# Optimization experiments

Measured on AMD Instinct MI355X. Metric: run time of the kernel, lower is better.

The kernel has to match this reference:

```python
import jax, jax.numpy as jnp
import numpy as np

NUM_HOPS = 3
SIGMA = 0.1
EPS = 1e-12  # torch F.normalize default eps


def setup_inputs() -> dict:
    key = jax.random.key(0)
    k1, k2 = jax.random.split(key)
    N, D, E = 50000, 128, 800000
    x = jax.random.normal(k1, (N, D), dtype=jnp.float32)
    edge_index = jax.random.randint(k2, (2, E), 0, N, dtype=jnp.int64)
    return {"x": x, "edge_index": edge_index}


def _l2_normalize(h):
    # matches torch.nn.functional.normalize(x, dim=1)
    n = jnp.linalg.norm(h, axis=1, keepdims=True)
    return h / jnp.maximum(n, EPS)


def reference(x, edge_index):
    N = x.shape[0]
    src, dst = edge_index[0], edge_index[1]
    noise_keys = jax.random.split(jax.random.key(1), NUM_HOPS)

    h = _l2_normalize(x)
    outs = [h]
    for k in range(NUM_HOPS):
        # edge-wise inner-product similarity + sigmoid gate
        e = jnp.sum(h[src] * h[dst], axis=1)          # [E]
        alpha = jax.nn.sigmoid(e)                     # [E]
        # sparse alpha^T @ h == segment-sum over dst of alpha * h[src]
        aggr = jax.ops.segment_sum(alpha[:, None] * h[src], dst, num_segments=N)  # [N, D]
        noised = aggr + SIGMA * jax.random.normal(noise_keys[k], aggr.shape, dtype=x.dtype)
        h = _l2_normalize(noised)
        outs.append(h)
    return jnp.stack(outs)                            # [NUM_HOPS+1, N, D]
```

## Files before the change

### kernel.cpp

```cpp
#include <hip/hip_runtime.h>
#include <cstdint>
#include <cstddef>

#define D 128

__host__ __device__ inline uint32_t rotl32(uint32_t v, int d) {
  return (v << d) | (v >> (32 - d));
}

__host__ __device__ inline void threefry2x32(uint32_t k0, uint32_t k1,
                                             uint32_t x0, uint32_t x1,
                                             uint32_t* o0, uint32_t* o1) {
  uint32_t k2 = k0 ^ k1 ^ 0x1BD11BDAu;
  x0 += k0; x1 += k1;
#define TF_RND(r) x0 += x1; x1 = rotl32(x1, (r)); x1 ^= x0;
  TF_RND(13) TF_RND(15) TF_RND(26) TF_RND(6)
  x0 += k1; x1 += k2 + 1u;
  TF_RND(17) TF_RND(29) TF_RND(16) TF_RND(24)
  x0 += k2; x1 += k0 + 2u;
  TF_RND(13) TF_RND(15) TF_RND(26) TF_RND(6)
  x0 += k0; x1 += k1 + 3u;
  TF_RND(17) TF_RND(29) TF_RND(16) TF_RND(24)
  x0 += k1; x1 += k2 + 4u;
  TF_RND(13) TF_RND(15) TF_RND(26) TF_RND(6)
  x0 += k2; x1 += k0 + 5u;
#undef TF_RND
  *o0 = x0; *o1 = x1;
}

__device__ inline float erfinv_f32(float x) {
  float w = -log1pf(-x * x);
  float p;
  if (w < 5.0f) {
    w = w - 2.5f;
    p = 2.81022636e-08f;
    p = fmaf(p, w, 3.43273939e-07f);
    p = fmaf(p, w, -3.5233877e-06f);
    p = fmaf(p, w, -4.39150654e-06f);
    p = fmaf(p, w, 0.00021858087f);
    p = fmaf(p, w, -0.00125372503f);
    p = fmaf(p, w, -0.00417768164f);
    p = fmaf(p, w, 0.246640727f);
    p = fmaf(p, w, 1.50140941f);
  } else {
    w = sqrtf(w) - 3.0f;
    p = -0.000200214257f;
    p = fmaf(p, w, 0.000100950558f);
    p = fmaf(p, w, 0.00134934322f);
    p = fmaf(p, w, -0.00367342844f);
    p = fmaf(p, w, 0.00573950773f);
    p = fmaf(p, w, -0.0076224613f);
    p = fmaf(p, w, 0.00943887047f);
    p = fmaf(p, w, 1.00167406f);
    p = fmaf(p, w, 2.83297682f);
  }
  return p * x;
}

__device__ inline float jax_normal_elem(uint32_t k0, uint32_t k1, uint32_t idx) {
  uint32_t o0, o1;
  threefry2x32(k0, k1, 0u, idx, &o0, &o1);
  uint32_t bits = o0 ^ o1;
  float f = __uint_as_float((bits >> 9) | 0x3F800000u) - 1.0f;
  float u = f * 2.0f + (-0.99999994f);
  u = fmaxf(-0.99999994f, u);
  return 1.41421356237309505f * erfinv_f32(u);
}

__device__ inline uint32_t f32_to_bf16_rne(float f) {
  uint32_t u = __float_as_uint(f);
  u += 0x7fffu + ((u >> 16) & 1u);
  return u >> 16;
}

__global__ __launch_bounds__(256) void hist4_kernel(
    const int* __restrict__ dst, int* __restrict__ counts,
    int* __restrict__ deg_hist, int E4, int E) {
  if (blockIdx.x == 0) {
    for (int b = threadIdx.x; b < 1024; b += 256) deg_hist[b] = 0;
  }
  int t = blockIdx.x * blockDim.x + threadIdx.x;
  if (t < E4) {
    int4 d = ((const int4*)dst)[t];
    atomicAdd(&counts[d.x], 1);
    atomicAdd(&counts[d.y], 1);
    atomicAdd(&counts[d.z], 1);
    atomicAdd(&counts[d.w], 1);
  }
  int rem = E4 * 4 + t;
  if (t < E - E4 * 4) atomicAdd(&counts[dst[rem]], 1);
}

__global__ __launch_bounds__(256) void scanA_kernel(
    int* __restrict__ counts, int* __restrict__ blocksums,
    int* __restrict__ deg, int* __restrict__ deg_hist, int N) {
  __shared__ int tmp[256];
  __shared__ int lhist[1024];
  for (int b = threadIdx.x; b < 1024; b += 256) lhist[b] = 0;
  int tid = threadIdx.x;
  int i = blockIdx.x * 256 + tid;
  int v = (i < N) ? counts[i] : 0;
  tmp[tid] = v;
  __syncthreads();
  if (i < N) {
    deg[i] = v;
    atomicAdd(&lhist[min(v, 1023)], 1);
  }
  for (int off = 1; off < 256; off <<= 1) {
    int t = (tid >= off) ? tmp[tid - off] : 0;
    __syncthreads();
    tmp[tid] += t;
    __syncthreads();
  }
  if (i < N) counts[i] = tmp[tid] - v;
  if (tid == 255) blocksums[blockIdx.x] = tmp[tid];
  __syncthreads();
  for (int b = threadIdx.x; b < 1024; b += 256) {
    int c = lhist[b];
    if (c) atomicAdd(&deg_hist[b], c);
  }
}

__global__ __launch_bounds__(256) void scanB_kernel(
    int* __restrict__ blocksums, int nb,
    const int* __restrict__ deg_hist, int* __restrict__ deg_cursor) {
  __shared__ int tmp[256];
  int tid = threadIdx.x;
  int v = (tid < nb) ? blocksums[tid] : 0;
  tmp[tid] = v;
  __syncthreads();
  for (int off = 1; off < 256; off <<= 1) {
    int t = (tid >= off) ? tmp[tid - off] : 0;
    __syncthreads();
    tmp[tid] += t;
    __syncthreads();
  }
  if (tid < nb) blocksums[tid] = tmp[tid] - v;
  __syncthreads();
  int loc[4], s = 0;
#pragma unroll
  for (int k = 0; k < 4; ++k) { loc[k] = deg_hist[tid * 4 + k]; s += loc[k]; }
  __syncthreads();
  tmp[tid] = s;
  __syncthreads();
  for (int off = 1; off < 256; off <<= 1) {
    int t = (tid >= off) ? tmp[tid - off] : 0;
    __syncthreads();
    tmp[tid] += t;
    __syncthreads();
  }
  int run = tmp[tid] - s;
#pragma unroll
  for (int k = 0; k < 4; ++k) { deg_cursor[tid * 4 + k] = run; run += loc[k]; }
}

__global__ __launch_bounds__(256) void scanC_kernel(
    int* __restrict__ offsets, int* __restrict__ cursor,
    const int* __restrict__ blocksums, const int* __restrict__ deg,
    int* __restrict__ deg_cursor, int* __restrict__ perm, int N, int E) {
  __shared__ int lhist[1024];
  __shared__ int lbase[1024];
  for (int b = threadIdx.x; b < 1024; b += 256) lhist[b] = 0;
  __syncthreads();
  int i = blockIdx.x * 256 + threadIdx.x;
  int d = 0, lpos = 0;
  if (i < N) {
    int o = offsets[i] + blocksums[blockIdx.x];
    offsets[i] = o;
    cursor[i] = o;
    d = min(deg[i], 1023);
    lpos = atomicAdd(&lhist[d], 1);
  }
  if (i == 0) offsets[N] = E;
  __syncthreads();
  for (int b = threadIdx.x; b < 1024; b += 256) {
    int c = lhist[b];
    lbase[b] = c ? atomicAdd(&deg_cursor[b], c) : 0;
  }
  __syncthreads();
  if (i < N) perm[lbase[d] + lpos] = i;
}

__global__ __launch_bounds__(256) void edgescatter4_kernel(
    const int* __restrict__ src, const int* __restrict__ dst,
    int* __restrict__ cursor, int* __restrict__ sorted_src, int E4, int E) {
  int t = blockIdx.x * blockDim.x + threadIdx.x;
  if (t < E4) {
    int4 d = ((const int4*)dst)[t];
    int4 s = ((const int4*)src)[t];
    sorted_src[atomicAdd(&cursor[d.x], 1)] = s.x;
    sorted_src[atomicAdd(&cursor[d.y], 1)] = s.y;
    sorted_src[atomicAdd(&cursor[d.z], 1)] = s.z;
    sorted_src[atomicAdd(&cursor[d.w], 1)] = s.w;
  }
  int rem = E4 * 4 + t;
  if (t < E - E4 * 4) {
    int d = dst[rem];
    sorted_src[atomicAdd(&cursor[d], 1)] = src[rem];
  }
}

__global__ __launch_bounds__(256) void norm_kernel(
    const float* __restrict__ in, float* __restrict__ out,
    uint16_t* __restrict__ mir, int N) {
  int t = blockIdx.x * blockDim.x + threadIdx.x;
  int row = t >> 6;
  int lane = t & 63;
  if (row >= N) return;
  size_t base = (size_t)row * D + 2 * lane;
  float2 v = *(const float2*)(in + base);
  float ss = v.x * v.x + v.y * v.y;
#pragma unroll
  for (int off = 32; off > 0; off >>= 1) ss += __shfl_xor(ss, off);
  float denom = fmaxf(sqrtf(ss), 1e-12f);
  float2 o = make_float2(v.x / denom, v.y / denom);
  *(float2*)(out + base) = o;
  if (mir) {
    uint32_t w = f32_to_bf16_rne(o.x) | (f32_to_bf16_rne(o.y) << 16);
    *(uint32_t*)(mir + base) = w;
  }
}

union V8 { float4 v[2]; float f[8]; };
union U4B { uint4 v; uint32_t u[4]; };

__device__ inline void hop_edge(const U4B& raw, const V8& b, V8& acc) {
  V8 af;
#pragma unroll
  for (int i = 0; i < 4; ++i) {
    af.f[2 * i] = __uint_as_float(raw.u[i] << 16);
    af.f[2 * i + 1] = __uint_as_float(raw.u[i] & 0xffff0000u);
  }
  float part = af.f[0] * b.f[0];
#pragma unroll
  for (int q = 1; q < 8; ++q) part = fmaf(af.f[q], b.f[q], part);
  part += __shfl_xor(part, 1);
  part += __shfl_xor(part, 2);
  part += __shfl_xor(part, 4);
  part += __shfl_xor(part, 8);
  float alpha = __builtin_amdgcn_rcpf(1.0f + __expf(-part));
#pragma unroll
  for (int q = 0; q < 8; ++q) acc.f[q] = fmaf(alpha, af.f[q], acc.f[q]);
}

__global__ __launch_bounds__(256, 4) void hop_kernel_bf16(
    const float* __restrict__ hprev, const uint16_t* __restrict__ mprev,
    float* __restrict__ hout, uint16_t* __restrict__ mout,
    const int* __restrict__ offsets, const int* __restrict__ sorted_src,
    const int* __restrict__ perm, int N, int E, uint32_t k0, uint32_t k1) {
  int g = (blockIdx.x * blockDim.x + threadIdx.x) >> 4;
  int sub = threadIdx.x & 15;
  if (g >= N) return;
  int r = perm[g];
  size_t rbase = (size_t)r * D + sub * 8;

  V8 b;
  {
    const float4* p = (const float4*)(hprev + rbase);
    b.v[0] = p[0]; b.v[1] = p[1];
  }
  V8 acc;
#pragma unroll
  for (int i = 0; i < 8; ++i) acc.f[i] = 0.f;

  int j0 = offsets[r];
  int cnt = offsets[r + 1] - j0;
  int Em1 = E - 1;
  const uint16_t* mp = mprev + sub * 8;

  U4B buf[4];
  int sNext[4];
#pragma unroll
  for (int q = 0; q < 4; ++q) {
    int s = sorted_src[min(j0 + q, Em1)];
    buf[q].v = *(const uint4*)(mp + (size_t)s * D);
  }
#pragma unroll
  for (int q = 0; q < 4; ++q) sNext[q] = sorted_src[min(j0 + 4 + q, Em1)];

  int cnt4 = cnt & ~3;
  int i = 0;
  for (; i < cnt4; i += 4) {
#pragma unroll
    for (int q = 0; q < 4; ++q) {
      hop_edge(buf[q], b, acc);
      buf[q].v = *(const uint4*)(mp + (size_t)sNext[q] * D);
      sNext[q] = sorted_src[min(j0 + i + 8 + q, Em1)];
    }
  }
  int rem = cnt - cnt4;
#pragma unroll
  for (int q = 0; q < 3; ++q)
    if (q < rem) hop_edge(buf[q], b, acc);

  uint32_t idx = (uint32_t)rbase;
  float ss = 0.f;
#pragma unroll
  for (int i2 = 0; i2 < 8; ++i2) {
    acc.f[i2] += 0.1f * jax_normal_elem(k0, k1, idx + (uint32_t)i2);
    ss = fmaf(acc.f[i2], acc.f[i2], ss);
  }
  ss += __shfl_xor(ss, 1);
  ss += __shfl_xor(ss, 2);
  ss += __shfl_xor(ss, 4);
  ss += __shfl_xor(ss, 8);
  float denom = fmaxf(sqrtf(ss), 1e-12f);
#pragma unroll
  for (int i2 = 0; i2 < 8; ++i2) acc.f[i2] = acc.f[i2] / denom;
  {
    float4* p = (float4*)(hout + rbase);
    p[0] = acc.v[0]; p[1] = acc.v[1];
  }
  if (mout) {
    U4B w;
#pragma unroll
    for (int i2 = 0; i2 < 4; ++i2)
      w.u[i2] = f32_to_bf16_rne(acc.f[2 * i2]) |
                (f32_to_bf16_rne(acc.f[2 * i2 + 1]) << 16);
    *(uint4*)(mout + rbase) = w.v;
  }
}

union V16 { float4 v[4]; float f[16]; };

__global__ __launch_bounds__(256) void hop_kernel_f32(
    const float* __restrict__ hprev, float* __restrict__ hout,
    const int* __restrict__ offsets, const int* __restrict__ sorted_src,
    const int* __restrict__ perm, int N, uint32_t k0, uint32_t k1) {
  int g = (blockIdx.x * blockDim.x + threadIdx.x) >> 3;
  int sub = threadIdx.x & 7;
  if (g >= N) return;
  int r = perm[g];
  size_t rbase = (size_t)r * D + sub * 16;

  V16 b;
  {
    const float4* p = (const float4*)(hprev + rbase);
    b.v[0] = p[0]; b.v[1] = p[1]; b.v[2] = p[2]; b.v[3] = p[3];
  }
  V16 acc;
#pragma unroll
  for (int i = 0; i < 16; ++i) acc.f[i] = 0.f;

  int j = offsets[r], jhi = offsets[r + 1];
  V16 a;
  if (j < jhi) {
    const float4* p = (const float4*)(hprev + (size_t)sorted_src[j] * D + sub * 16);
    a.v[0] = p[0]; a.v[1] = p[1]; a.v[2] = p[2]; a.v[3] = p[3];
  }
  while (j < jhi) {
    int jn = j + 1;
    V16 an;
    if (jn < jhi) {
      const float4* p = (const float4*)(hprev + (size_t)sorted_src[jn] * D + sub * 16);
      an.v[0] = p[0]; an.v[1] = p[1]; an.v[2] = p[2]; an.v[3] = p[3];
    }
    float part = a.f[0] * b.f[0];
#pragma unroll
    for (int i = 1; i < 16; ++i) part = fmaf(a.f[i], b.f[i], part);
    part += __shfl_xor(part, 1);
    part += __shfl_xor(part, 2);
    part += __shfl_xor(part, 4);
    float alpha = 1.0f / (1.0f + expf(-part));
#pragma unroll
    for (int i = 0; i < 16; ++i) acc.f[i] = fmaf(alpha, a.f[i], acc.f[i]);
    a = an;
    j = jn;
  }

  uint32_t idx = (uint32_t)rbase;
  float ss = 0.f;
#pragma unroll
  for (int i = 0; i < 16; ++i) {
    acc.f[i] += 0.1f * jax_normal_elem(k0, k1, idx + (uint32_t)i);
    ss = fmaf(acc.f[i], acc.f[i], ss);
  }
  ss += __shfl_xor(ss, 1);
  ss += __shfl_xor(ss, 2);
  ss += __shfl_xor(ss, 4);
  float denom = fmaxf(sqrtf(ss), 1e-12f);
#pragma unroll
  for (int i = 0; i < 16; ++i) acc.f[i] = acc.f[i] / denom;
  {
    float4* p = (float4*)(hout + rbase);
    p[0] = acc.v[0]; p[1] = acc.v[1]; p[2] = acc.v[2]; p[3] = acc.v[3];
  }
}

extern "C" void kernel_launch(void* const* d_in, const int* in_sizes, int n_in,
                              void* d_out, int out_size, void* d_ws, size_t ws_size,
                              hipStream_t stream) {
  const float* x = (const float*)d_in[0];
  const int* ei = (const int*)d_in[1];
  int N = in_sizes[0] / D;
  int E = in_sizes[1] / 2;
  const int* src = ei;
  const int* dst = ei + E;
  float* out = (float*)d_out;
  size_t ND = (size_t)N * D;

  int nblocksN = (N + 255) / 256;

  int* offsets = (int*)d_ws;
  int* cursor = offsets + (N + 1);
  int* perm = cursor + N;
  int* deg = perm + N;
  int* deg_hist = deg + N;
  int* deg_cursor = deg_hist + 1024;
  int* blocksums = deg_cursor + 1024;
  int* sorted_src = blocksums + 256;
  size_t intWords = (size_t)(N + 1) + N + N + N + 1024 + 1024 + 256 + E;
  size_t mirOff = (intWords * 4 + 255) & ~(size_t)255;
  size_t need = mirOff + 2 * ND * sizeof(uint16_t);
  bool use_bf16 = ws_size >= need;
  uint16_t* mir0 = (uint16_t*)((char*)d_ws + mirOff);
  uint16_t* mir1 = mir0 + ND;

  uint32_t nk0[3], nk1[3];
  for (int k = 0; k < 3; ++k)
    threefry2x32(0u, 1u, 0u, (uint32_t)k, &nk0[k], &nk1[k]);

  int E4 = E / 4;
  int e4Blocks = (max(E4, E - E4 * 4) + 255) / 256;
  int rowWaveBlocks = (int)(((size_t)N * 64 + 255) / 256);
  int hopBlocks16 = (int)(((size_t)N * 16 + 255) / 256);
  int hopBlocks8 = (int)(((size_t)N * 8 + 255) / 256);

  hipMemsetAsync(offsets, 0, (size_t)(N + 1) * sizeof(int), stream);
  hipLaunchKernelGGL(hist4_kernel, dim3(e4Blocks), dim3(256), 0, stream,
                     dst, offsets, deg_hist, E4, E);
  hipLaunchKernelGGL(scanA_kernel, dim3(nblocksN), dim3(256), 0, stream,
                     offsets, blocksums, deg, deg_hist, N);
  hipLaunchKernelGGL(scanB_kernel, dim3(1), dim3(256), 0, stream,
                     blocksums, nblocksN, deg_hist, deg_cursor);
  hipLaunchKernelGGL(scanC_kernel, dim3(nblocksN), dim3(256), 0, stream,
                     offsets, cursor, blocksums, deg, deg_cursor, perm, N, E);
  hipLaunchKernelGGL(edgescatter4_kernel, dim3(e4Blocks), dim3(256), 0, stream,
                     src, dst, cursor, sorted_src, E4, E);

  hipLaunchKernelGGL(norm_kernel, dim3(rowWaveBlocks), dim3(256), 0, stream,
                     x, out, use_bf16 ? mir0 : (uint16_t*)nullptr, N);

  if (use_bf16) {
    uint16_t* mirs[4] = {mir0, mir1, mir0, nullptr};
    for (int k = 0; k < 3; ++k) {
      const float* hk = out + (size_t)k * ND;
      float* hk1 = out + (size_t)(k + 1) * ND;
      hipLaunchKernelGGL(hop_kernel_bf16, dim3(hopBlocks16), dim3(256), 0, stream,
                         hk, mirs[k], hk1, mirs[k + 1], offsets, sorted_src,
                         perm, N, E, nk0[k], nk1[k]);
    }
  } else {
    for (int k = 0; k < 3; ++k) {
      const float* hk = out + (size_t)k * ND;
      float* hk1 = out + (size_t)(k + 1) * ND;
      hipLaunchKernelGGL(hop_kernel_f32, dim3(hopBlocks8), dim3(256), 0, stream,
                         hk, hk1, offsets, sorted_src, perm, N, nk0[k], nk1[k]);
    }
  }
}
```

Baseline: 390.0 us.

## Fuse input normalization into histogram kernel and micro-optimize bf16 hop kernel

```diff
diff --git a/kernel.cpp b/kernel.cpp
--- a/kernel.cpp
+++ b/kernel.cpp
@@ -3,6 +3,8 @@
 #include <cstddef>
 
 #define D 128
+
+typedef float v2f __attribute__((ext_vector_type(2)));
 
 __host__ __device__ inline uint32_t rotl32(uint32_t v, int d) {
   return (v << d) | (v >> (32 - d));
@@ -57,6 +59,36 @@
   return p * x;
 }
 
+__device__ inline float erfinv_fast(float x) {
+  float t = fmaf(-x, x, 1.0f);
+  float w = -0.693147180559945f * __builtin_amdgcn_logf(t);
+  float p;
+  if (__builtin_expect(w < 5.0f, 1)) {
+    w = w - 2.5f;
+    p = 2.81022636e-08f;
+    p = fmaf(p, w, 3.43273939e-07f);
+    p = fmaf(p, w, -3.5233877e-06f);
+    p = fmaf(p, w, -4.39150654e-06f);
+    p = fmaf(p, w, 0.00021858087f);
+    p = fmaf(p, w, -0.00125372503f);
+    p = fmaf(p, w, -0.00417768164f);
+    p = fmaf(p, w, 0.246640727f);
+    p = fmaf(p, w, 1.50140941f);
+  } else {
+    w = __builtin_amdgcn_sqrtf(w) - 3.0f;
+    p = -0.000200214257f;
+    p = fmaf(p, w, 0.000100950558f);
+    p = fmaf(p, w, 0.00134934322f);
+    p = fmaf(p, w, -0.00367342844f);
+    p = fmaf(p, w, 0.00573950773f);
+    p = fmaf(p, w, -0.0076224613f);
+    p = fmaf(p, w, 0.00943887047f);
+    p = fmaf(p, w, 1.00167406f);
+    p = fmaf(p, w, 2.83297682f);
+  }
+  return p * x;
+}
+
 __device__ inline float jax_normal_elem(uint32_t k0, uint32_t k1, uint32_t idx) {
   uint32_t o0, o1;
   threefry2x32(k0, k1, 0u, idx, &o0, &o1);
@@ -67,28 +99,60 @@
   return 1.41421356237309505f * erfinv_f32(u);
 }
 
+__device__ inline float jax_normal_fast(uint32_t k0, uint32_t k1, uint32_t idx) {
+  uint32_t o0, o1;
+  threefry2x32(k0, k1, 0u, idx, &o0, &o1);
+  uint32_t bits = o0 ^ o1;
+  float f = __uint_as_float((bits >> 9) | 0x3F800000u) - 1.0f;
+  float u = f * 2.0f + (-0.99999994f);
+  u = fmaxf(-0.99999994f, u);
+  return 1.41421356237309505f * erfinv_fast(u);
+}
+
 __device__ inline uint32_t f32_to_bf16_rne(float f) {
   uint32_t u = __float_as_uint(f);
   u += 0x7fffu + ((u >> 16) & 1u);
   return u >> 16;
 }
 
-__global__ __launch_bounds__(256) void hist4_kernel(
+__global__ __launch_bounds__(256) void front_kernel(
     const int* __restrict__ dst, int* __restrict__ counts,
-    int* __restrict__ deg_hist, int E4, int E) {
-  if (blockIdx.x == 0) {
-    for (int b = threadIdx.x; b < 1024; b += 256) deg_hist[b] = 0;
-  }
-  int t = blockIdx.x * blockDim.x + threadIdx.x;
-  if (t < E4) {
-    int4 d = ((const int4*)dst)[t];
-    atomicAdd(&counts[d.x], 1);
-    atomicAdd(&counts[d.y], 1);
-    atomicAdd(&counts[d.z], 1);
-    atomicAdd(&counts[d.w], 1);
-  }
-  int rem = E4 * 4 + t;
-  if (t < E - E4 * 4) atomicAdd(&counts[dst[rem]], 1);
+    int* __restrict__ deg_hist, int E4, int E,
+    const float* __restrict__ xin, float* __restrict__ out0,
+    uint16_t* __restrict__ mir, int N, int nbHist) {
+  int w = blockIdx.x;
+  if (w < nbHist) {
+    if (w == 0) {
+      for (int bb = threadIdx.x; bb < 1024; bb += 256) deg_hist[bb] = 0;
+    }
+    int t = w * 256 + threadIdx.x;
+    if (t < E4) {
+      int4 d4 = ((const int4*)dst)[t];
+      atomicAdd(&counts[d4.x], 1);
+      atomicAdd(&counts[d4.y], 1);
+      atomicAdd(&counts[d4.z], 1);
+      atomicAdd(&counts[d4.w], 1);
+    }
+    int rem = E4 * 4 + t;
+    if (t < E - E4 * 4) atomicAdd(&counts[dst[rem]], 1);
+    return;
+  }
+  int t = (w - nbHist) * 256 + threadIdx.x;
+  int row = t >> 6;
+  int lane = t & 63;
+  if (row >= N) return;
+  size_t base = (size_t)row * D + 2 * lane;
+  float2 v = *(const float2*)(xin + base);
+  float ss = v.x * v.x + v.y * v.y;
+#pragma unroll
+  for (int off = 32; off > 0; off >>= 1) ss += __shfl_xor(ss, off);
+  float denom = fmaxf(sqrtf(ss), 1e-12f);
+  float2 o = make_float2(v.x / denom, v.y / denom);
+  *(float2*)(out0 + base) = o;
+  if (mir) {
+    uint32_t wq = f32_to_bf16_rne(o.x) | (f32_to_bf16_rne(o.y) << 16);
+    *(uint32_t*)(mir + base) = wq;
+  }
 }
 
 __global__ __launch_bounds__(256) void scanA_kernel(
@@ -200,50 +264,31 @@
   }
 }
 
-__global__ __launch_bounds__(256) void norm_kernel(
-    const float* __restrict__ in, float* __restrict__ out,
-    uint16_t* __restrict__ mir, int N) {
-  int t = blockIdx.x * blockDim.x + threadIdx.x;
-  int row = t >> 6;
-  int lane = t & 63;
-  if (row >= N) return;
-  size_t base = (size_t)row * D + 2 * lane;
-  float2 v = *(const float2*)(in + base);
-  float ss = v.x * v.x + v.y * v.y;
-#pragma unroll
-  for (int off = 32; off > 0; off >>= 1) ss += __shfl_xor(ss, off);
-  float denom = fmaxf(sqrtf(ss), 1e-12f);
-  float2 o = make_float2(v.x / denom, v.y / denom);
-  *(float2*)(out + base) = o;
-  if (mir) {
-    uint32_t w = f32_to_bf16_rne(o.x) | (f32_to_bf16_rne(o.y) << 16);
-    *(uint32_t*)(mir + base) = w;
-  }
-}
-
-union V8 { float4 v[2]; float f[8]; };
+union V8 { float4 v[2]; v2f d[4]; float f[8]; };
 union U4B { uint4 v; uint32_t u[4]; };
 
-__device__ inline void hop_edge(const U4B& raw, const V8& b, V8& acc) {
+__device__ inline void hop_edge_pk(const U4B& raw, const V8& b, V8& acc) {
   V8 af;
 #pragma unroll
   for (int i = 0; i < 4; ++i) {
     af.f[2 * i] = __uint_as_float(raw.u[i] << 16);
     af.f[2 * i + 1] = __uint_as_float(raw.u[i] & 0xffff0000u);
   }
-  float part = af.f[0] * b.f[0];
-#pragma unroll
-  for (int q = 1; q < 8; ++q) part = fmaf(af.f[q], b.f[q], part);
+  v2f p2 = af.d[0] * b.d[0];
+#pragma unroll
+  for (int q = 1; q < 4; ++q) p2 = __builtin_elementwise_fma(af.d[q], b.d[q], p2);
+  float part = p2.x + p2.y;
   part += __shfl_xor(part, 1);
   part += __shfl_xor(part, 2);
   part += __shfl_xor(part, 4);
   part += __shfl_xor(part, 8);
   float alpha = __builtin_amdgcn_rcpf(1.0f + __expf(-part));
-#pragma unroll
-  for (int q = 0; q < 8; ++q) acc.f[q] = fmaf(alpha, af.f[q], acc.f[q]);
-}
-
-__global__ __launch_bounds__(256, 4) void hop_kernel_bf16(
+  v2f av = { alpha, alpha };
+#pragma unroll
+  for (int q = 0; q < 4; ++q) acc.d[q] = __builtin_elementwise_fma(av, af.d[q], acc.d[q]);
+}
+
+__global__ __launch_bounds__(256, 8) void hop_kernel_bf16(
     const float* __restrict__ hprev, const uint16_t* __restrict__ mprev,
     float* __restrict__ hout, uint16_t* __restrict__ mout,
     const int* __restrict__ offsets, const int* __restrict__ sorted_src,
@@ -266,38 +311,37 @@
   int j0 = offsets[r];
   int cnt = offsets[r + 1] - j0;
   int Em1 = E - 1;
-  const uint16_t* mp = mprev + sub * 8;
+  const char* mb = (const char*)mprev + (uint32_t)(sub * 16);
 
   U4B buf[4];
   int sNext[4];
 #pragma unroll
   for (int q = 0; q < 4; ++q) {
-    int s = sorted_src[min(j0 + q, Em1)];
-    buf[q].v = *(const uint4*)(mp + (size_t)s * D);
+    uint32_t s = (uint32_t)sorted_src[min(j0 + q, Em1)];
+    buf[q].v = *(const uint4*)(mb + (s << 8));
   }
 #pragma unroll
   for (int q = 0; q < 4; ++q) sNext[q] = sorted_src[min(j0 + 4 + q, Em1)];
 
   int cnt4 = cnt & ~3;
-  int i = 0;
-  for (; i < cnt4; i += 4) {
+  for (int i = 0; i < cnt4; i += 4) {
 #pragma unroll
     for (int q = 0; q < 4; ++q) {
-      hop_edge(buf[q], b, acc);
-      buf[q].v = *(const uint4*)(mp + (size_t)sNext[q] * D);
+      hop_edge_pk(buf[q], b, acc);
+      buf[q].v = *(const uint4*)(mb + ((uint32_t)sNext[q] << 8));
       sNext[q] = sorted_src[min(j0 + i + 8 + q, Em1)];
     }
   }
   int rem = cnt - cnt4;
 #pragma unroll
   for (int q = 0; q < 3; ++q)
-    if (q < rem) hop_edge(buf[q], b, acc);
+    if (q < rem) hop_edge_pk(buf[q], b, acc);
 
   uint32_t idx = (uint32_t)rbase;
   float ss = 0.f;
 #pragma unroll
   for (int i2 = 0; i2 < 8; ++i2) {
-    acc.f[i2] += 0.1f * jax_normal_elem(k0, k1, idx + (uint32_t)i2);
+    acc.f[i2] += 0.1f * jax_normal_fast(k0, k1, idx + (uint32_t)i2);
     ss = fmaf(acc.f[i2], acc.f[i2], ss);
   }
   ss += __shfl_xor(ss, 1);
@@ -305,19 +349,21 @@
   ss += __shfl_xor(ss, 4);
   ss += __shfl_xor(ss, 8);
   float denom = fmaxf(sqrtf(ss), 1e-12f);
-#pragma unroll
-  for (int i2 = 0; i2 < 8; ++i2) acc.f[i2] = acc.f[i2] / denom;
+  float inv = __builtin_amdgcn_rcpf(denom);
+  inv = inv * fmaf(-denom, inv, 2.0f);
+#pragma unroll
+  for (int i2 = 0; i2 < 8; ++i2) acc.f[i2] *= inv;
   {
     float4* p = (float4*)(hout + rbase);
     p[0] = acc.v[0]; p[1] = acc.v[1];
   }
   if (mout) {
-    U4B w;
+    U4B wq;
 #pragma unroll
     for (int i2 = 0; i2 < 4; ++i2)
-      w.u[i2] = f32_to_bf16_rne(acc.f[2 * i2]) |
-                (f32_to_bf16_rne(acc.f[2 * i2 + 1]) << 16);
-    *(uint4*)(mout + rbase) = w.v;
+      wq.u[i2] = f32_to_bf16_rne(acc.f[2 * i2]) |
+                 (f32_to_bf16_rne(acc.f[2 * i2 + 1]) << 16);
+    *(uint4*)(mout + rbase) = wq.v;
   }
 }
 
@@ -411,8 +457,8 @@
   int* sorted_src = blocksums + 256;
   size_t intWords = (size_t)(N + 1) + N + N + N + 1024 + 1024 + 256 + E;
   size_t mirOff = (intWords * 4 + 255) & ~(size_t)255;
-  size_t need = mirOff + 2 * ND * sizeof(uint16_t);
-  bool use_bf16 = ws_size >= need;
+  size_t needMir = mirOff + 2 * ND * sizeof(uint16_t);
+  bool use_bf16 = ws_size >= needMir;
   uint16_t* mir0 = (uint16_t*)((char*)d_ws + mirOff);
   uint16_t* mir1 = mir0 + ND;
 
@@ -427,8 +473,9 @@
   int hopBlocks8 = (int)(((size_t)N * 8 + 255) / 256);
 
   hipMemsetAsync(offsets, 0, (size_t)(N + 1) * sizeof(int), stream);
-  hipLaunchKernelGGL(hist4_kernel, dim3(e4Blocks), dim3(256), 0, stream,
-                     dst, offsets, deg_hist, E4, E);
+  hipLaunchKernelGGL(front_kernel, dim3(e4Blocks + rowWaveBlocks), dim3(256), 0,
+                     stream, dst, offsets, deg_hist, E4, E,
+                     x, out, use_bf16 ? mir0 : (uint16_t*)nullptr, N, e4Blocks);
   hipLaunchKernelGGL(scanA_kernel, dim3(nblocksN), dim3(256), 0, stream,
                      offsets, blocksums, deg, deg_hist, N);
   hipLaunchKernelGGL(scanB_kernel, dim3(1), dim3(256), 0, stream,
@@ -438,17 +485,14 @@
   hipLaunchKernelGGL(edgescatter4_kernel, dim3(e4Blocks), dim3(256), 0, stream,
                      src, dst, cursor, sorted_src, E4, E);
 
-  hipLaunchKernelGGL(norm_kernel, dim3(rowWaveBlocks), dim3(256), 0, stream,
-                     x, out, use_bf16 ? mir0 : (uint16_t*)nullptr, N);
-
   if (use_bf16) {
     uint16_t* mirs[4] = {mir0, mir1, mir0, nullptr};
     for (int k = 0; k < 3; ++k) {
       const float* hk = out + (size_t)k * ND;
       float* hk1 = out + (size_t)(k + 1) * ND;
-      hipLaunchKernelGGL(hop_kernel_bf16, dim3(hopBlocks16), dim3(256), 0, stream,
-                         hk, mirs[k], hk1, mirs[k + 1], offsets, sorted_src,
-                         perm, N, E, nk0[k], nk1[k]);
+      hipLaunchKernelGGL(hop_kernel_bf16, dim3(hopBlocks16), dim3(256), 0,
+                         stream, hk, mirs[k], hk1, mirs[k + 1], offsets,
+                         sorted_src, perm, N, E, nk0[k], nk1[k]);
     }
   } else {
     for (int k = 0; k < 3; ++k) {
```

Measured after the change: 347.6 us. 1.12x faster.
